# Kernel tuning notes

Hardware: AMD Instinct MI355X
Metric: run time of the kernel (lower is better)

The kernel has to match this reference:

```python
import jax, jax.numpy as jnp
import numpy as np

EPS = 1e-5

def _ln(x, g, b):
    m = jnp.mean(x, axis=-1, keepdims=True)
    v = jnp.var(x, axis=-1, keepdims=True)
    return (x - m) * jax.lax.rsqrt(v + EPS) * g + b

def _gelu(x):
    return jax.nn.gelu(x, approximate=False)  # torch nn.GELU default is exact erf

def setup_inputs() -> dict:
    key = jax.random.key(0)
    B, N, D, H = 4, 1024, 128, 12
    HID = H * D
    ks = jax.random.split(key, 16)
    s = lambda k, sh, fan: jax.random.normal(k, sh, jnp.float32) * (fan ** -0.5)
    return {
        "x": jax.random.normal(ks[0], (B, N, D), jnp.float32),
        # project: LN(D) -> Linear(D,HID) -> GELU -> Linear(HID,HID)
        "ln1_g": jnp.ones((D,), jnp.float32), "ln1_b": jnp.zeros((D,), jnp.float32),
        "W1": s(ks[1], (D, HID), D), "b1": jnp.zeros((HID,), jnp.float32),
        "W2": s(ks[2], (HID, HID), HID), "b2": jnp.zeros((HID,), jnp.float32),
        # shared Attention(inc=D, outc=D)
        "aln_g": jnp.ones((D,), jnp.float32), "aln_b": jnp.zeros((D,), jnp.float32),
        "Wqkv": s(ks[3], (D, 3 * D), D), "bqkv": jnp.zeros((3 * D,), jnp.float32),
        "Wl": s(ks[4], (D, D), D), "bl": jnp.zeros((D,), jnp.float32),
        # out_proj: LN(HID) -> Linear(HID, D) -> GELU
        "lno_g": jnp.ones((HID,), jnp.float32), "lno_b": jnp.zeros((HID,), jnp.float32),
        "Wo": s(ks[5], (HID, D), HID), "bo": jnp.zeros((D,), jnp.float32),
    }

def reference(x, ln1_g, ln1_b, W1, b1, W2, b2,
              aln_g, aln_b, Wqkv, bqkv, Wl, bl,
              lno_g, lno_b, Wo, bo):
    B, N, D = x.shape
    # project (dropout is identity in eval mode)
    h = _ln(x, ln1_g, ln1_b)
    h = _gelu(h @ W1 + b1)
    h = h @ W2 + b2                      # [B, N, H*D]
    H = h.shape[-1] // D
    # chunk along last dim into H features of width D; fold heads into batch
    f = h.reshape(B, N, H, D).transpose(0, 2, 1, 3).reshape(B * H, N, D)
    # shared Attention applied to each head-chunk
    a = _ln(f, aln_g, aln_b)
    qkv = a @ Wqkv + bqkv
    q, k, v = jnp.split(qkv, 3, axis=-1)
    scores = jax.nn.softmax(jnp.einsum('bnd,bmd->bnm', q, k) * (D ** -0.5), axis=-1)
    o = jnp.einsum('bnm,bmd->bnd', scores, v)
    o = o @ Wl + bl
    o = _gelu(o + f)                     # [B*H, N, D]
    # concat heads back along last dim
    feats = o.reshape(B, H, N, D).transpose(0, 2, 1, 3).reshape(B, N, H * D)
    out = _gelu(_ln(feats, lno_g, lno_b) @ Wo + bo)
    return out
```

## Files before the change

kernel.cpp:

```cpp
#include <hip/hip_runtime.h>
#include <stdint.h>

typedef unsigned short u16;
typedef __attribute__((ext_vector_type(8))) short short8;
typedef __attribute__((ext_vector_type(4))) float floatx4;

__device__ inline float b2f(u16 u) {
  union { uint32_t i; float f; } x; x.i = ((uint32_t)u) << 16; return x.f;
}
__device__ inline u16 f2b(float f) {
  union { float f; uint32_t i; } x; x.f = f;
  uint32_t r = (x.i + 0x7FFFu + ((x.i >> 16) & 1u)) >> 16;
  return (u16)r;
}
__device__ inline float gelu_f(float v) {
  return 0.5f * v * (1.0f + erff(v * 0.70710678118654752440f));
}

#define MFMA16(a, b, c) __builtin_amdgcn_mfma_f32_16x16x32_bf16((a), (b), (c), 0, 0, 0)

__device__ __forceinline__ void gl2lds16(const u16* g, u16* l) {
  __builtin_amdgcn_global_load_lds(
      (const __attribute__((address_space(1))) uint32_t*)(uintptr_t)g,
      (__attribute__((address_space(3))) uint32_t*)(uint32_t)(uintptr_t)l,
      16, 0, 0);
}

__global__ __launch_bounds__(256)
void tpose_all_kernel(const float* __restrict__ W1, const float* __restrict__ W2,
                      const float* __restrict__ Wqkv, const float* __restrict__ Wl,
                      const float* __restrict__ Wo,
                      u16* __restrict__ w1t, u16* __restrict__ w2t,
                      u16* __restrict__ wqkvt, u16* __restrict__ wlt,
                      u16* __restrict__ wot) {
  int id = blockIdx.x;
  const float* src; u16* dst; int R, C, bx, by;
  if (id < 2304)      { src = W2;   dst = w2t;   R = 1536; C = 1536; bx = (id % 48) * 32; by = (id / 48) * 32; }
  else if (id < 2496) { id -= 2304; src = W1;   dst = w1t;   R = 128;  C = 1536; bx = (id % 48) * 32; by = (id / 48) * 32; }
  else if (id < 2688) { id -= 2496; src = Wo;   dst = wot;   R = 1536; C = 128;  bx = (id % 4) * 32;  by = (id / 4) * 32; }
  else if (id < 2736) { id -= 2688; src = Wqkv; dst = wqkvt; R = 128;  C = 384;  bx = (id % 12) * 32; by = (id / 12) * 32; }
  else                { id -= 2736; src = Wl;   dst = wlt;   R = 128;  C = 128;  bx = (id % 4) * 32;  by = (id / 4) * 32; }
  __shared__ u16 t[32][33];
  int tx = threadIdx.x & 31, ty = threadIdx.x >> 5;
  for (int i = 0; i < 32; i += 8)
    t[ty + i][tx] = f2b(src[(size_t)(by + ty + i) * C + bx + tx]);
  __syncthreads();
  for (int i = 0; i < 32; i += 8)
    dst[(size_t)(bx + ty + i) * R + by + tx] = t[tx][ty + i];
}

__global__ __launch_bounds__(256)
void ln128_f32_kernel(const float* __restrict__ X, const float* __restrict__ g,
                      const float* __restrict__ bb, u16* __restrict__ Y) {
  int tid = threadIdx.x, w = tid >> 6, lane = tid & 63;
  int row = blockIdx.x * 4 + w;
  const float* xr = X + (size_t)row * 128;
  float2 xv = *(const float2*)(xr + lane * 2);
  float x0 = xv.x, x1 = xv.y;
  float s = x0 + x1, s2 = x0 * x0 + x1 * x1;
  for (int m = 1; m < 64; m <<= 1) { s += __shfl_xor(s, m, 64); s2 += __shfl_xor(s2, m, 64); }
  float mean = s * (1.0f / 128.0f);
  float var = s2 * (1.0f / 128.0f) - mean * mean;
  float rstd = 1.0f / sqrtf(var + 1e-5f);
  float2 gv = *(const float2*)(g + lane * 2);
  float2 bv = *(const float2*)(bb + lane * 2);
  float y0 = (x0 - mean) * rstd * gv.x + bv.x;
  float y1 = (x1 - mean) * rstd * gv.y + bv.y;
  *(uint32_t*)(Y + (size_t)row * 128 + lane * 2) =
      (uint32_t)f2b(y0) | ((uint32_t)f2b(y1) << 16);
}

__global__ __launch_bounds__(256)
void ln128_perm_kernel(const u16* __restrict__ X, const float* __restrict__ g,
                       const float* __restrict__ bb, u16* __restrict__ Y) {
  int tid = threadIdx.x, w = tid >> 6, lane = tid & 63;
  int rid = blockIdx.x * 4 + w;
  int bh = rid >> 10, n = rid & 1023;
  int b = bh / 12, h = bh % 12;
  const u16* xr = X + ((size_t)(b * 1024 + n)) * 1536 + h * 128;
  uint32_t u = *(const uint32_t*)(xr + lane * 2);
  float x0 = b2f(u & 0xffff), x1 = b2f(u >> 16);
  float s = x0 + x1, s2 = x0 * x0 + x1 * x1;
  for (int m = 1; m < 64; m <<= 1) { s += __shfl_xor(s, m, 64); s2 += __shfl_xor(s2, m, 64); }
  float mean = s * (1.0f / 128.0f);
  float var = s2 * (1.0f / 128.0f) - mean * mean;
  float rstd = 1.0f / sqrtf(var + 1e-5f);
  float2 gv = *(const float2*)(g + lane * 2);
  float2 bv = *(const float2*)(bb + lane * 2);
  float y0 = (x0 - mean) * rstd * gv.x + bv.x;
  float y1 = (x1 - mean) * rstd * gv.y + bv.y;
  *(uint32_t*)(Y + (size_t)rid * 128 + lane * 2) =
      (uint32_t)f2b(y0) | ((uint32_t)f2b(y1) << 16);
}

__global__ __launch_bounds__(256)
void ln1536_kernel(const u16* __restrict__ X, const float* __restrict__ g,
                   const float* __restrict__ bb, u16* __restrict__ Y) {
  int row = blockIdx.x, tid = threadIdx.x;
  const u16* xr = X + (size_t)row * 1536;
  uint32_t u0 = *(const uint32_t*)(xr + tid * 6);
  uint32_t u1 = *(const uint32_t*)(xr + tid * 6 + 2);
  uint32_t u2 = *(const uint32_t*)(xr + tid * 6 + 4);
  float v[6] = { b2f(u0 & 0xffff), b2f(u0 >> 16), b2f(u1 & 0xffff),
                 b2f(u1 >> 16),    b2f(u2 & 0xffff), b2f(u2 >> 16) };
  float s = 0.f, s2 = 0.f;
  for (int j = 0; j < 6; j++) { s += v[j]; s2 += v[j] * v[j]; }
  for (int m = 1; m < 64; m <<= 1) { s += __shfl_xor(s, m, 64); s2 += __shfl_xor(s2, m, 64); }
  __shared__ float red[8];
  int w = tid >> 6, lane = tid & 63;
  if (lane == 0) { red[w] = s; red[4 + w] = s2; }
  __syncthreads();
  s = red[0] + red[1] + red[2] + red[3];
  s2 = red[4] + red[5] + red[6] + red[7];
  float mean = s * (1.0f / 1536.0f);
  float var = s2 * (1.0f / 1536.0f) - mean * mean;
  float rstd = 1.0f / sqrtf(var + 1e-5f);
  uint32_t o[3];
  for (int p = 0; p < 3; p++) {
    int c = tid * 6 + p * 2;
    float y0 = (v[p * 2] - mean) * rstd * g[c] + bb[c];
    float y1 = (v[p * 2 + 1] - mean) * rstd * g[c + 1] + bb[c + 1];
    o[p] = (uint32_t)f2b(y0) | ((uint32_t)f2b(y1) << 16);
  }
  u16* yr = Y + (size_t)row * 1536 + tid * 6;
  *(uint32_t*)(yr) = o[0];
  *(uint32_t*)(yr + 2) = o[1];
  *(uint32_t*)(yr + 4) = o[2];
}

__global__ __launch_bounds__(256)
void qkv_kernel(const u16* __restrict__ A, const u16* __restrict__ BT,
                const float* __restrict__ bias, u16* __restrict__ qkv,
                u16* __restrict__ vT) {
  const int K = 128;
  __shared__ __align__(16) u16 abuf[128 * 32];
  __shared__ __align__(16) u16 bbuf[128 * 32];
  int tid = threadIdx.x;
  int w = tid >> 6, lane = tid & 63, ln = lane & 15, quad = lane >> 4;
  int bm = blockIdx.x * 128, bn = blockIdx.y * 128;
  int wr = w >> 1, wc = w & 1;
  floatx4 acc[4][4] = {};
  for (int k0 = 0; k0 < K; k0 += 32) {
    __syncthreads();
    for (int rd = 0; rd < 2; rd++) {
      int c = tid + rd * 256;
      int row = c >> 2, col = (c & 3) * 8;
      gl2lds16(A + (size_t)(bm + row) * K + k0 + col, abuf + c * 8);
      gl2lds16(BT + (size_t)(bn + row) * K + k0 + col, bbuf + c * 8);
    }
    __syncthreads();
    short8 af[4], bf[4];
    for (int i = 0; i < 4; i++)
      af[i] = *(const short8*)(abuf + (wr * 64 + i * 16 + ln) * 32 + quad * 8);
    for (int j = 0; j < 4; j++)
      bf[j] = *(const short8*)(bbuf + (wc * 64 + j * 16 + ln) * 32 + quad * 8);
    for (int i = 0; i < 4; i++)
      for (int j = 0; j < 4; j++)
        acc[i][j] = MFMA16(af[i], bf[j], acc[i][j]);
  }
  if (blockIdx.y < 2) {
    for (int i = 0; i < 4; i++) {
      int row0 = bm + wr * 64 + i * 16 + quad * 4;
      for (int j = 0; j < 4; j++) {
        int col = bn + wc * 64 + j * 16 + ln;
        float bv = bias[col];
        for (int r = 0; r < 4; r++)
          qkv[(size_t)(row0 + r) * 256 + col] = f2b(acc[i][j][r] + bv);
      }
    }
  } else {
    int bh = bm >> 10;
    int nb = bm & 1023;
    u16* vp = vT + (size_t)bh * 128 * 1024;
    for (int i = 0; i < 4; i++) {
      int n0 = nb + wr * 64 + i * 16 + quad * 4;
      for (int j = 0; j < 4; j++) {
        int d = wc * 64 + j * 16 + ln;
        float bv = bias[256 + d];
        u16 tmp[4];
        for (int r = 0; r < 4; r++) tmp[r] = f2b(acc[i][j][r] + bv);
        *(uint2*)(vp + (size_t)d * 1024 + n0) = *(const uint2*)tmp;
      }
    }
  }
}

template <int GELU, int RES, typename OUTT>
__global__ __launch_bounds__(256)
void gemm64_kernel(const u16* __restrict__ A, const u16* __restrict__ BT,
                   const float* __restrict__ bias, const u16* __restrict__ res,
                   OUTT* __restrict__ C, int M, int N, int K) {
  __shared__ __align__(16) u16 abuf[64 * 32];
  __shared__ __align__(16) u16 bbuf[128 * 32];
  int tid = threadIdx.x;
  int w = tid >> 6, lane = tid & 63, ln = lane & 15, quad = lane >> 4;
  int bm = blockIdx.x * 64, bn = blockIdx.y * 128;
  floatx4 acc[4][2] = {};
  for (int k0 = 0; k0 < K; k0 += 32) {
    __syncthreads();
    for (int rd = 0; rd < 2; rd++) {
      int c = tid + rd * 256;
      int row = c >> 2, col = (c & 3) * 8;
      gl2lds16(BT + (size_t)(bn + row) * K + k0 + col, bbuf + c * 8);
    }
    {
      int c = tid;
      int row = c >> 2, col = (c & 3) * 8;
      gl2lds16(A + (size_t)(bm + row) * K + k0 + col, abuf + c * 8);
    }
    __syncthreads();
    short8 af[4], bf[2];
    for (int i = 0; i < 4; i++)
      af[i] = *(const short8*)(abuf + (i * 16 + ln) * 32 + quad * 8);
    for (int j = 0; j < 2; j++)
      bf[j] = *(const short8*)(bbuf + (w * 32 + j * 16 + ln) * 32 + quad * 8);
    for (int i = 0; i < 4; i++)
      for (int j = 0; j < 2; j++)
        acc[i][j] = MFMA16(af[i], bf[j], acc[i][j]);
  }
  for (int i = 0; i < 4; i++) {
    int row0 = bm + i * 16 + quad * 4;
    for (int j = 0; j < 2; j++) {
      int col = bn + w * 32 + j * 16 + ln;
      float bv = bias[col];
      for (int r = 0; r < 4; r++) {
        float v = acc[i][j][r] + bv;
        if (RES) v += b2f(res[(size_t)(row0 + r) * N + col]);
        if (GELU) v = gelu_f(v);
        if constexpr (sizeof(OUTT) == 2)
          C[(size_t)(row0 + r) * N + col] = f2b(v);
        else
          C[(size_t)(row0 + r) * N + col] = v;
      }
    }
  }
}

template <int GELU, int RES, typename OUTT>
__global__ __launch_bounds__(256)
void gemm64b_kernel(const u16* __restrict__ A, const u16* __restrict__ BT,
                    const float* __restrict__ bias, const u16* __restrict__ res,
                    OUTT* __restrict__ C, int M, int N, int K) {
  __shared__ __align__(16) u16 abuf[2 * 64 * 32];
  __shared__ __align__(16) u16 bbuf[2 * 128 * 32];
  int tid = threadIdx.x;
  int w = tid >> 6, lane = tid & 63, ln = lane & 15, quad = lane >> 4;
  int bm = blockIdx.x * 64, bn = blockIdx.y * 128;
  floatx4 acc[4][2] = {};
  for (int k0 = 0; k0 < K; k0 += 64) {
    __syncthreads();
    for (int ks = 0; ks < 2; ks++) {
      {
        int c = tid;
        int row = c >> 2, cc = c & 3;
        gl2lds16(A + (size_t)(bm + row) * K + k0 + ks * 32 + cc * 8,
                 abuf + ks * 2048 + c * 8);
      }
      for (int rd = 0; rd < 2; rd++) {
        int c = tid + rd * 256;
        int row = c >> 2, cc = c & 3;
        gl2lds16(BT + (size_t)(bn + row) * K + k0 + ks * 32 + cc * 8,
                 bbuf + ks * 4096 + c * 8);
      }
    }
    __syncthreads();
    short8 af[2][4], bf[2][2];
    for (int ks = 0; ks < 2; ks++) {
      for (int i = 0; i < 4; i++)
        af[ks][i] = *(const short8*)(abuf + ks * 2048 + (i * 16 + ln) * 32 + quad * 8);
      for (int j = 0; j < 2; j++)
        bf[ks][j] = *(const short8*)(bbuf + ks * 4096 + (w * 32 + j * 16 + ln) * 32 + quad * 8);
    }
    for (int i = 0; i < 4; i++)
      for (int j = 0; j < 2; j++) {
        acc[i][j] = MFMA16(af[0][i], bf[0][j], acc[i][j]);
        acc[i][j] = MFMA16(af[1][i], bf[1][j], acc[i][j]);
      }
  }
  for (int i = 0; i < 4; i++) {
    int row0 = bm + i * 16 + quad * 4;
    for (int j = 0; j < 2; j++) {
      int col = bn + w * 32 + j * 16 + ln;
      float bv = bias[col];
      for (int r = 0; r < 4; r++) {
        float v = acc[i][j][r] + bv;
        if (RES) v += b2f(res[(size_t)(row0 + r) * N + col]);
        if (GELU) v = gelu_f(v);
        if constexpr (sizeof(OUTT) == 2)
          C[(size_t)(row0 + r) * N + col] = f2b(v);
        else
          C[(size_t)(row0 + r) * N + col] = v;
      }
    }
  }
}

__global__ __launch_bounds__(256)
void gemmwl_kernel(const u16* __restrict__ A, const u16* __restrict__ BT,
                   const float* __restrict__ bias, const u16* __restrict__ res,
                   u16* __restrict__ feats) {
  const int K = 128;
  __shared__ __align__(16) u16 abuf[64 * 32];
  __shared__ __align__(16) u16 bbuf[128 * 32];
  int tid = threadIdx.x;
  int w = tid >> 6, lane = tid & 63, ln = lane & 15, quad = lane >> 4;
  int bm = blockIdx.x * 64;
  floatx4 acc[4][2] = {};
  for (int k0 = 0; k0 < K; k0 += 32) {
    __syncthreads();
    for (int rd = 0; rd < 2; rd++) {
      int c = tid + rd * 256;
      int row = c >> 2, col = (c & 3) * 8;
      gl2lds16(BT + (size_t)row * K + k0 + col, bbuf + c * 8);
    }
    {
      int c = tid;
      int row = c >> 2, col = (c & 3) * 8;
      gl2lds16(A + (size_t)(bm + row) * K + k0 + col, abuf + c * 8);
    }
    __syncthreads();
    short8 af[4], bf[2];
    for (int i = 0; i < 4; i++)
      af[i] = *(const short8*)(abuf + (i * 16 + ln) * 32 + quad * 8);
    for (int j = 0; j < 2; j++)
      bf[j] = *(const short8*)(bbuf + (w * 32 + j * 16 + ln) * 32 + quad * 8);
    for (int i = 0; i < 4; i++)
      for (int j = 0; j < 2; j++)
        acc[i][j] = MFMA16(af[i], bf[j], acc[i][j]);
  }
  int bh = bm >> 10, nb = bm & 1023;
  int b = bh / 12, hh = bh % 12;
  size_t obase = ((size_t)b * 1024) * 1536 + hh * 128;
  for (int i = 0; i < 4; i++) {
    int n0 = nb + i * 16 + quad * 4;
    for (int j = 0; j < 2; j++) {
      int col = w * 32 + j * 16 + ln;
      float bv = bias[col];
      for (int r = 0; r < 4; r++) {
        size_t idx = obase + (size_t)(n0 + r) * 1536 + col;
        float v = acc[i][j][r] + bv + b2f(res[idx]);
        feats[idx] = f2b(gelu_f(v));
      }
    }
  }
}

__global__ __launch_bounds__(256)
void gemm64_part_kernel(const u16* __restrict__ A, const u16* __restrict__ BT,
                        float* __restrict__ pws, int Kfull, int kspan) {
  __shared__ __align__(16) u16 abuf[64 * 32];
  __shared__ __align__(16) u16 bbuf[128 * 32];
  int tid = threadIdx.x;
  int w = tid >> 6, lane = tid & 63, ln = lane & 15, quad = lane >> 4;
  int bm = blockIdx.x * 64;
  int kbeg = blockIdx.y * kspan, kend = kbeg + kspan;
  float* Cp = pws + (size_t)blockIdx.y * 4096 * 128;
  floatx4 acc[4][2] = {};
  for (int k0 = kbeg; k0 < kend; k0 += 32) {
    __syncthreads();
    for (int rd = 0; rd < 2; rd++) {
      int c = tid + rd * 256;
      int row = c >> 2, col = (c & 3) * 8;
      gl2lds16(BT + (size_t)row * Kfull + k0 + col, bbuf + c * 8);
    }
    {
      int c = tid;
      int row = c >> 2, col = (c & 3) * 8;
      gl2lds16(A + (size_t)(bm + row) * Kfull + k0 + col, abuf + c * 8);
    }
    __syncthreads();
    short8 af[4], bf[2];
    for (int i = 0; i < 4; i++)
      af[i] = *(const short8*)(abuf + (i * 16 + ln) * 32 + quad * 8);
    for (int j = 0; j < 2; j++)
      bf[j] = *(const short8*)(bbuf + (w * 32 + j * 16 + ln) * 32 + quad * 8);
    for (int i = 0; i < 4; i++)
      for (int j = 0; j < 2; j++)
        acc[i][j] = MFMA16(af[i], bf[j], acc[i][j]);
  }
  for (int i = 0; i < 4; i++) {
    int row0 = bm + i * 16 + quad * 4;
    for (int j = 0; j < 2; j++) {
      int col = w * 32 + j * 16 + ln;
      for (int r = 0; r < 4; r++)
        Cp[(size_t)(row0 + r) * 128 + col] = acc[i][j][r];
    }
  }
}

__global__ __launch_bounds__(256)
void combine_wo_kernel(const float* __restrict__ p, const float* __restrict__ bias,
                       float* __restrict__ out) {
  int i = blockIdx.x * 256 + threadIdx.x;
  const int SZ = 4096 * 128;
  float v = p[i] + p[i + SZ] + p[i + 2 * SZ] + p[i + 3 * SZ] + bias[i & 127];
  out[i] = gelu_f(v);
}

__global__ __launch_bounds__(256)
void attn_kernel(const u16* __restrict__ qkv, const u16* __restrict__ vT,
                 u16* __restrict__ obuf) {
  int blk = blockIdx.x;
  int xcd = blk & 7, slot = blk >> 3;
  int bh = xcd * 6 + (slot >> 4);
  int qt = slot & 15;
  int tid = threadIdx.x, w = tid >> 6, lane = tid & 63, ln = lane & 15, quad = lane >> 4;
  __shared__ __align__(16) u16 kbuf[4 * 64 * 32];
  __shared__ __align__(16) u16 vbuf[2 * 128 * 32];
  __shared__ __align__(16) u16 pbuf[4][16 * 72];
  const int rs = 256;
  size_t base = (size_t)bh * 1024 * 256;
  const u16* qp = qkv + base;
  const u16* kp = qkv + base + 128;
  const u16* vp = vT + (size_t)bh * 128 * 1024;

  short8 onesb;
  {
    short v = (ln == 0) ? (short)0x3F80 : (short)0;
    for (int j = 0; j < 8; j++) onesb[j] = v;
  }

  int qrow = qt * 64 + w * 16 + ln;
  short8 qf[4];
  for (int st = 0; st < 4; st++)
    qf[st] = *(const short8*)(qp + (size_t)qrow * rs + st * 32 + quad * 8);

  floatx4 o[9] = {};
  const float K2 = 0.08838834764831845f * 1.4426950408889634f;

  for (int kt = 0; kt < 16; kt++) {
    __syncthreads();
    for (int it = 0; it < 4; it++) {
      int c = it * 256 + tid;
      int st = c >> 8, key = (c >> 2) & 63, cc = c & 3;
      gl2lds16(kp + (size_t)(kt * 64 + key) * rs + st * 32 + cc * 8, kbuf + c * 8);
      int kf = c >> 9, d = (c >> 2) & 127;
      gl2lds16(vp + (size_t)d * 1024 + kt * 64 + kf * 32 + cc * 8, vbuf + c * 8);
    }
    __syncthreads();

    floatx4 s[4] = {};
    for (int t = 0; t < 4; t++)
      for (int st = 0; st < 4; st++) {
        short8 bk = *(const short8*)(kbuf + st * 2048 + (t * 16 + ln) * 32 + quad * 8);
        s[t] = MFMA16(qf[st], bk, s[t]);
      }
    for (int r = 0; r < 4; r++) {
      int prow = (quad * 4 + r) * 72;
      pbuf[w][prow + ln]      = f2b(exp2f(s[0][r] * K2));
      pbuf[w][prow + 16 + ln] = f2b(exp2f(s[1][r] * K2));
      pbuf[w][prow + 32 + ln] = f2b(exp2f(s[2][r] * K2));
      pbuf[w][prow + 48 + ln] = f2b(exp2f(s[3][r] * K2));
    }
    for (int kf = 0; kf < 2; kf++) {
      short8 ap = *(const short8*)(&pbuf[w][ln * 72 + kf * 32 + quad * 8]);
      for (int dt = 0; dt < 8; dt++) {
        short8 bv = *(const short8*)(vbuf + kf * 4096 + (dt * 16 + ln) * 32 + quad * 8);
        o[dt] = MFMA16(ap, bv, o[dt]);
      }
      o[8] = MFMA16(ap, onesb, o[8]);
    }
  }

  for (int r = 0; r < 4; r++) {
    float l = __shfl(o[8][r], lane & 48);
    float inv = 1.0f / l;
    int n = qt * 64 + w * 16 + quad * 4 + r;
    size_t ob = ((size_t)bh * 1024 + n) * 128;
    for (int dt = 0; dt < 8; dt++)
      obuf[ob + dt * 16 + ln] = f2b(o[dt][r] * inv);
  }
}

extern "C" void kernel_launch(void* const* d_in, const int* in_sizes, int n_in,
                              void* d_out, int out_size, void* d_ws, size_t ws_size,
                              hipStream_t stream) {
  (void)in_sizes; (void)n_in; (void)out_size; (void)ws_size;
  const float* x    = (const float*)d_in[0];
  const float* ln1g = (const float*)d_in[1];
  const float* ln1b = (const float*)d_in[2];
  const float* W1   = (const float*)d_in[3];
  const float* b1   = (const float*)d_in[4];
  const float* W2   = (const float*)d_in[5];
  const float* b2   = (const float*)d_in[6];
  const float* alng = (const float*)d_in[7];
  const float* alnb = (const float*)d_in[8];
  const float* Wqkv = (const float*)d_in[9];
  const float* bqkv = (const float*)d_in[10];
  const float* Wl   = (const float*)d_in[11];
  const float* bl   = (const float*)d_in[12];
  const float* lnog = (const float*)d_in[13];
  const float* lnob = (const float*)d_in[14];
  const float* Wo   = (const float*)d_in[15];
  const float* bo   = (const float*)d_in[16];
  float* out = (float*)d_out;

  char* ws = (char*)d_ws;
  size_t off = 0;
  auto alloc = [&](size_t elems) { u16* p = (u16*)(ws + off); off += elems * sizeof(u16); return p; };
  u16* w1t   = alloc((size_t)1536 * 128);
  u16* w2t   = alloc((size_t)1536 * 1536);
  u16* wqkvt = alloc((size_t)384 * 128);
  u16* wlt   = alloc((size_t)128 * 128);
  u16* wot   = alloc((size_t)128 * 1536);
  u16* lnx   = alloc((size_t)4096 * 128);
  u16* h1    = alloc((size_t)4096 * 1536);
  u16* h2    = alloc((size_t)4096 * 1536);
  u16* aln   = alloc((size_t)49152 * 128);
  u16* qkv   = alloc((size_t)49152 * 256);
  u16* obuf  = alloc((size_t)49152 * 128);
  u16* vT = h1;
  u16* feats = aln;
  u16* lnf = qkv;
  float* pws = (float*)h1;

  dim3 T(256);
  tpose_all_kernel<<<dim3(2752), T, 0, stream>>>(W1, W2, Wqkv, Wl, Wo,
                                                 w1t, w2t, wqkvt, wlt, wot);
  ln128_f32_kernel<<<dim3(4096 / 4), T, 0, stream>>>(x, ln1g, ln1b, lnx);
  gemm64_kernel<1, 0, u16><<<dim3(4096 / 64, 1536 / 128), T, 0, stream>>>(
      lnx, w1t, b1, nullptr, h1, 4096, 1536, 128);
  gemm64b_kernel<0, 0, u16><<<dim3(4096 / 64, 1536 / 128), T, 0, stream>>>(
      h1, w2t, b2, nullptr, h2, 4096, 1536, 1536);
  ln128_perm_kernel<<<dim3(49152 / 4), T, 0, stream>>>(h2, alng, alnb, aln);
  qkv_kernel<<<dim3(49152 / 128, 3), T, 0, stream>>>(aln, wqkvt, bqkv, qkv, vT);
  attn_kernel<<<dim3(768), T, 0, stream>>>(qkv, vT, obuf);
  gemmwl_kernel<<<dim3(49152 / 64), T, 0, stream>>>(obuf, wlt, bl, h2, feats);
  ln1536_kernel<<<dim3(4096), T, 0, stream>>>(feats, lnog, lnob, lnf);
  gemm64_part_kernel<<<dim3(4096 / 64, 4), T, 0, stream>>>(lnf, wot, pws, 1536, 384);
  combine_wo_kernel<<<dim3(4096 * 128 / 256), T, 0, stream>>>(pws, bo, out);
}
```

Baseline: 255.2 us.

## Split attention keys across wave pairs and keep P in registers via transposed MFMA

Each wave now handles 32 query rows over half of each 64-key tile, computing S transposed (K as A operand) so that the exponentiated probabilities can be packed straight into MFMA B fragments with v_cvt_pk_bf16_f32. This removes the LDS round trip for P and replaces the ones-column MFMA row-sum with a register accumulation. The two key-halves' partial outputs and sums are merged through LDS at the end, and launch bounds request 3 blocks per CU. The cost is more accumulator registers (two sets of 8 output tiles) and an extra LDS reduction in the epilogue.

```diff
diff --git a/kernel.cpp b/kernel.cpp
--- a/kernel.cpp
+++ b/kernel.cpp
@@ -397,7 +397,7 @@
   out[i] = gelu_f(v);
 }
 
-__global__ __launch_bounds__(256)
+__global__ __launch_bounds__(256, 3)
 void attn_kernel(const u16* __restrict__ qkv, const u16* __restrict__ vT,
                  u16* __restrict__ obuf) {
   int blk = blockIdx.x;
@@ -405,27 +405,25 @@
   int bh = xcd * 6 + (slot >> 4);
   int qt = slot & 15;
   int tid = threadIdx.x, w = tid >> 6, lane = tid & 63, ln = lane & 15, quad = lane >> 4;
-  __shared__ __align__(16) u16 kbuf[4 * 64 * 32];
-  __shared__ __align__(16) u16 vbuf[2 * 128 * 32];
-  __shared__ __align__(16) u16 pbuf[4][16 * 72];
+  int pair = w & 1, half = w >> 1;
+  __shared__ __align__(16) u16 smem[16384 + 128];
+  u16* kbuf = smem;
+  u16* vbuf = smem + 8192;
   const int rs = 256;
   size_t base = (size_t)bh * 1024 * 256;
   const u16* qp = qkv + base;
   const u16* kp = qkv + base + 128;
   const u16* vp = vT + (size_t)bh * 128 * 1024;
 
-  short8 onesb;
-  {
-    short v = (ln == 0) ? (short)0x3F80 : (short)0;
-    for (int j = 0; j < 8; j++) onesb[j] = v;
-  }
-
-  int qrow = qt * 64 + w * 16 + ln;
-  short8 qf[4];
-  for (int st = 0; st < 4; st++)
-    qf[st] = *(const short8*)(qp + (size_t)qrow * rs + st * 32 + quad * 8);
-
-  floatx4 o[9] = {};
+  short8 qf[2][4];
+  for (int g = 0; g < 2; g++) {
+    int qrow = qt * 64 + pair * 32 + g * 16 + ln;
+    for (int st = 0; st < 4; st++)
+      qf[g][st] = *(const short8*)(qp + (size_t)qrow * rs + st * 32 + quad * 8);
+  }
+
+  floatx4 o[2][8] = {};
+  float lsum[2] = {0.f, 0.f};
   const float K2 = 0.08838834764831845f * 1.4426950408889634f;
 
   for (int kt = 0; kt < 16; kt++) {
@@ -439,36 +437,77 @@
     }
     __syncthreads();
 
-    floatx4 s[4] = {};
-    for (int t = 0; t < 4; t++)
+    floatx4 s[2][2] = {};
+    for (int tt = 0; tt < 2; tt++)
       for (int st = 0; st < 4; st++) {
-        short8 bk = *(const short8*)(kbuf + st * 2048 + (t * 16 + ln) * 32 + quad * 8);
-        s[t] = MFMA16(qf[st], bk, s[t]);
-      }
-    for (int r = 0; r < 4; r++) {
-      int prow = (quad * 4 + r) * 72;
-      pbuf[w][prow + ln]      = f2b(exp2f(s[0][r] * K2));
-      pbuf[w][prow + 16 + ln] = f2b(exp2f(s[1][r] * K2));
-      pbuf[w][prow + 32 + ln] = f2b(exp2f(s[2][r] * K2));
-      pbuf[w][prow + 48 + ln] = f2b(exp2f(s[3][r] * K2));
-    }
-    for (int kf = 0; kf < 2; kf++) {
-      short8 ap = *(const short8*)(&pbuf[w][ln * 72 + kf * 32 + quad * 8]);
+        short8 kv = *(const short8*)(kbuf + st * 2048 +
+                                     ((half * 2 + tt) * 16 + ln) * 32 + quad * 8);
+        s[0][tt] = MFMA16(kv, qf[0][st], s[0][tt]);
+        s[1][tt] = MFMA16(kv, qf[1][st], s[1][tt]);
+      }
+
+    short8 pfrag[2];
+    for (int g = 0; g < 2; g++) {
+      float p0[4], p1[4];
+      for (int r = 0; r < 4; r++) {
+        p0[r] = exp2f(s[g][0][r] * K2);
+        p1[r] = exp2f(s[g][1][r] * K2);
+        lsum[g] += p0[r] + p1[r];
+      }
+      uint32_t a0, a1, b0, b1;
+      asm("v_cvt_pk_bf16_f32 %0, %1, %2" : "=v"(a0) : "v"(p0[0]), "v"(p0[1]));
+      asm("v_cvt_pk_bf16_f32 %0, %1, %2" : "=v"(a1) : "v"(p0[2]), "v"(p0[3]));
+      asm("v_cvt_pk_bf16_f32 %0, %1, %2" : "=v"(b0) : "v"(p1[0]), "v"(p1[1]));
+      asm("v_cvt_pk_bf16_f32 %0, %1, %2" : "=v"(b1) : "v"(p1[2]), "v"(p1[3]));
+      union { uint32_t u[4]; short8 v; } pu;
+      pu.u[0] = a0; pu.u[1] = a1; pu.u[2] = b0; pu.u[3] = b1;
+      pfrag[g] = pu.v;
+    }
+
+    for (int dt = 0; dt < 8; dt++) {
+      const u16* vrow = vbuf + half * 4096 + (dt * 16 + ln) * 32 + quad * 4;
+      union { uint2 d2[2]; short8 v; } av;
+      av.d2[0] = *(const uint2*)(vrow);
+      av.d2[1] = *(const uint2*)(vrow + 16);
+      o[0][dt] = MFMA16(av.v, pfrag[0], o[0][dt]);
+      o[1][dt] = MFMA16(av.v, pfrag[1], o[1][dt]);
+    }
+  }
+
+  for (int g = 0; g < 2; g++) {
+    lsum[g] += __shfl_xor(lsum[g], 16, 64);
+    lsum[g] += __shfl_xor(lsum[g], 32, 64);
+  }
+
+  __syncthreads();
+  float* mbuf = (float*)smem;
+  float* lbuf = (float*)(smem + 16384);
+  if (half == 1) {
+    float* mp = mbuf + pair * 4096;
+    for (int g = 0; g < 2; g++)
+      for (int dt = 0; dt < 8; dt++)
+        for (int r = 0; r < 4; r++)
+          mp[(dt * 16 + quad * 4 + r) * 32 + g * 16 + ln] = o[g][dt][r];
+    if (quad == 0) {
+      lbuf[pair * 32 + ln] = lsum[0];
+      lbuf[pair * 32 + 16 + ln] = lsum[1];
+    }
+  }
+  __syncthreads();
+  if (half == 0) {
+    float* mp = mbuf + pair * 4096;
+    for (int g = 0; g < 2; g++) {
+      float lt = lsum[g] + lbuf[pair * 32 + g * 16 + ln];
+      float inv = 1.0f / lt;
+      int n = qt * 64 + pair * 32 + g * 16 + ln;
+      size_t ob = ((size_t)bh * 1024 + n) * 128;
       for (int dt = 0; dt < 8; dt++) {
-        short8 bv = *(const short8*)(vbuf + kf * 4096 + (dt * 16 + ln) * 32 + quad * 8);
-        o[dt] = MFMA16(ap, bv, o[dt]);
-      }
-      o[8] = MFMA16(ap, onesb, o[8]);
-    }
-  }
-
-  for (int r = 0; r < 4; r++) {
-    float l = __shfl(o[8][r], lane & 48);
-    float inv = 1.0f / l;
-    int n = qt * 64 + w * 16 + quad * 4 + r;
-    size_t ob = ((size_t)bh * 1024 + n) * 128;
-    for (int dt = 0; dt < 8; dt++)
-      obuf[ob + dt * 16 + ln] = f2b(o[dt][r] * inv);
+        u16 tmp[4];
+        for (int r = 0; r < 4; r++)
+          tmp[r] = f2b((o[g][dt][r] + mp[(dt * 16 + quad * 4 + r) * 32 + g * 16 + ln]) * inv);
+        *(uint2*)(obuf + ob + dt * 16 + quad * 4) = *(const uint2*)tmp;
+      }
+    }
   }
 }
 
```

Measured after the change: 269.6 us. 1.06x slower.
